# Kernel tuning notes

Hardware: AMD Instinct MI355X
Metric: run time of the kernel (lower is better)

The kernel has to match this reference:

```python
import jax, jax.numpy as jnp
import numpy as np

TEMPERATURE = 1.0
WEIGHT = 1.0


def _transitivity_sum(rel):
    """rel: [N, N] relation probabilities for one (batch, relation) slice.
    Computes sum_{a,b,c} relu(rel[a,b] - rel[a,c] * rel[b,c]) via a scan over c
    (outer product of column c), keeping memory at O(N^2) instead of O(N^3)."""
    def step(acc, col):  # col = rel[:, c], shape [N]
        viol = jax.nn.relu(rel - col[:, None] * col[None, :])  # [N, N]
        return acc + jnp.sum(viol), None
    acc, _ = jax.lax.scan(step, jnp.zeros((), rel.dtype), rel.T)
    return acc


def setup_inputs() -> dict:
    key = jax.random.key(0)
    B, N, R = 2, 512, 4
    relation_logits = jax.random.normal(key, (B, N, N, R), dtype=jnp.float32)
    entity_masks = jnp.ones((B, N), dtype=jnp.int32)
    return {"relation_logits": relation_logits, "entity_masks": entity_masks}


def reference(relation_logits, entity_masks):
    B, N, _, R = relation_logits.shape
    probs = jax.nn.sigmoid(relation_logits / TEMPERATURE)  # [B, N, N, R]
    m = (entity_masks > 0).astype(probs.dtype)             # [B, N]
    rel = probs * m[:, :, None, None] * m[:, None, :, None]
    # flatten (batch, relation) and vmap the per-matrix cubic reduction
    rel_br = jnp.transpose(rel, (0, 3, 1, 2)).reshape(B * R, N, N)
    per = jax.vmap(_transitivity_sum)(rel_br)              # [B*R]
    # per-batch loss = sum_r / R; final = weight * mean over batch
    return WEIGHT * jnp.sum(per) / (R * B)
```

## Files before the change

kernel.cpp:

```cpp
#include <hip/hip_runtime.h>
#include <math.h>

#define N      512
#define RNUM   4
#define BNUM   2
#define NSLICE (RNUM * BNUM)
#define TILE   64
#define CT     64
#define PAD    4
#define STRIDE (TILE + PAD)
#define CSPLIT 2

__device__ __forceinline__ float sigmoidf_(float x) {
  return 1.0f / (1.0f + __expf(-x));
}

__global__ void zero_out_kernel(float* out) { out[0] = 0.0f; }

__global__ __launch_bounds__(256) void prep_kernel(const float* __restrict__ logits,
                                                   const int* __restrict__ masks,
                                                   float* __restrict__ P) {
  int t = blockIdx.x * 256 + threadIdx.x;
  int b = t / (N * N);
  int rem = t - b * (N * N);
  int i = rem / N;
  int j = rem - i * N;
  float4 lg = *(const float4*)(logits + (size_t)t * 4);
  float mm = ((masks[b * N + i] > 0) && (masks[b * N + j] > 0)) ? 1.0f : 0.0f;
  size_t base = (size_t)b * RNUM * N * N + rem;
  P[base + 0 * (size_t)N * N] = mm * sigmoidf_(lg.x);
  P[base + 1 * (size_t)N * N] = mm * sigmoidf_(lg.y);
  P[base + 2 * (size_t)N * N] = mm * sigmoidf_(lg.z);
  P[base + 3 * (size_t)N * N] = mm * sigmoidf_(lg.w);
}

template <bool USE_P>
__global__ __launch_bounds__(256, 4) void trans_main_kernel(const float* __restrict__ P,
                                                            const float* __restrict__ logits,
                                                            const int* __restrict__ masks,
                                                            float* __restrict__ out) {
  const int zz = blockIdx.z;
  const int s  = zz / CSPLIT;
  const int cz = zz % CSPLIT;
  const int a0 = blockIdx.y * TILE;
  const int b0 = blockIdx.x * TILE;
  const int bb = s >> 2;
  const int r  = s & 3;
  const int cbeg = cz * (N / CSPLIT);
  const int cend = cbeg + (N / CSPLIT);

  __shared__ __align__(16) float tA[CT][STRIDE];
  __shared__ __align__(16) float tB[CT][STRIDE];
  __shared__ float wsum[4];

  const int tid = threadIdx.x;
  const int ta  = tid & 15;
  const int tb  = tid >> 4;

  const float* Ps  = P + (size_t)s * N * N;
  const int* mrow  = masks + bb * N;

  float rab[4][4];
  if (USE_P) {
#pragma unroll
    for (int x = 0; x < 4; ++x) {
      float4 rr = *(const float4*)(Ps + (size_t)(a0 + ta * 4 + x) * N + b0 + tb * 4);
      rab[x][0] = rr.x; rab[x][1] = rr.y; rab[x][2] = rr.z; rab[x][3] = rr.w;
    }
  } else {
    float ma[4], mb[4];
#pragma unroll
    for (int x = 0; x < 4; ++x) ma[x] = (mrow[a0 + ta * 4 + x] > 0) ? 1.0f : 0.0f;
#pragma unroll
    for (int y = 0; y < 4; ++y) mb[y] = (mrow[b0 + tb * 4 + y] > 0) ? 1.0f : 0.0f;
#pragma unroll
    for (int x = 0; x < 4; ++x)
#pragma unroll
      for (int y = 0; y < 4; ++y) {
        size_t idx = ((size_t)(bb * N + a0 + ta * 4 + x) * N + (b0 + tb * 4 + y)) * RNUM + r;
        rab[x][y] = sigmoidf_(logits[idx]) * ma[x] * mb[y];
      }
  }

  float acc[4][4];
#pragma unroll
  for (int x = 0; x < 4; ++x)
#pragma unroll
    for (int y = 0; y < 4; ++y) acc[x][y] = 0.0f;

  for (int c0 = cbeg; c0 < cend; c0 += CT) {
    __syncthreads();
    if (USE_P) {
#pragma unroll
      for (int it = 0; it < 4; ++it) {
        int f  = it * 256 + tid;
        int c4 = f & 15;
        int i  = f >> 4;
        int pcol = (((i >> 2) ^ c4) << 2) | (i & 3);
        float4 va = *(const float4*)(Ps + (size_t)(a0 + i) * N + c0 + c4 * 4);
        tA[c4 * 4 + 0][pcol] = va.x;
        tA[c4 * 4 + 1][pcol] = va.y;
        tA[c4 * 4 + 2][pcol] = va.z;
        tA[c4 * 4 + 3][pcol] = va.w;
        float4 vb = *(const float4*)(Ps + (size_t)(b0 + i) * N + c0 + c4 * 4);
        tB[c4 * 4 + 0][pcol] = vb.x;
        tB[c4 * 4 + 1][pcol] = vb.y;
        tB[c4 * 4 + 2][pcol] = vb.z;
        tB[c4 * 4 + 3][pcol] = vb.w;
      }
    } else {
#pragma unroll
      for (int it = 0; it < 16; ++it) {
        int e = it * 256 + tid;
        int c = e & 63;
        int i = e >> 6;
        int pcol = (((i >> 2) ^ ((c >> 2) & 15)) << 2) | (i & 3);
        float mc = (mrow[c0 + c] > 0) ? 1.0f : 0.0f;
        {
          float mi = (mrow[a0 + i] > 0) ? 1.0f : 0.0f;
          size_t idx = ((size_t)(bb * N + a0 + i) * N + (c0 + c)) * RNUM + r;
          tA[c][pcol] = sigmoidf_(logits[idx]) * mi * mc;
        }
        {
          float mi = (mrow[b0 + i] > 0) ? 1.0f : 0.0f;
          size_t idx = ((size_t)(bb * N + b0 + i) * N + (c0 + c)) * RNUM + r;
          tB[c][pcol] = sigmoidf_(logits[idx]) * mi * mc;
        }
      }
    }
    __syncthreads();

#pragma unroll 4
    for (int cg = 0; cg < CT / 4; ++cg) {
      const float* pa = &tA[cg * 4][(ta ^ cg) << 2];
      const float* pb = &tB[cg * 4][(tb ^ cg) << 2];
#pragma unroll
      for (int dc = 0; dc < 4; ++dc) {
        float4 va4 = *(const float4*)(pa + dc * STRIDE);
        float4 vb4 = *(const float4*)(pb + dc * STRIDE);
        float av[4] = {va4.x, va4.y, va4.z, va4.w};
        float bv[4] = {vb4.x, vb4.y, vb4.z, vb4.w};
#pragma unroll
        for (int x = 0; x < 4; ++x)
#pragma unroll
          for (int y = 0; y < 4; ++y) {
            float v = fmaf(-av[x], bv[y], rab[x][y]);
            acc[x][y] += fmaxf(v, 0.0f);
          }
      }
    }
  }

  float tsum = 0.0f;
#pragma unroll
  for (int x = 0; x < 4; ++x)
#pragma unroll
    for (int y = 0; y < 4; ++y) tsum += acc[x][y];

  for (int off = 32; off > 0; off >>= 1) tsum += __shfl_down(tsum, off, 64);

  const int wid  = tid >> 6;
  const int lane = tid & 63;
  if (lane == 0) wsum[wid] = tsum;
  __syncthreads();
  if (tid == 0) {
    float bsum = wsum[0] + wsum[1] + wsum[2] + wsum[3];
    atomicAdd(out, bsum * 0.125f);
  }
}

extern "C" void kernel_launch(void* const* d_in, const int* in_sizes, int n_in,
                              void* d_out, int out_size, void* d_ws, size_t ws_size,
                              hipStream_t stream) {
  const float* logits = (const float*)d_in[0];
  const int*   masks  = (const int*)d_in[1];
  float*       out    = (float*)d_out;

  const size_t P_BYTES = (size_t)NSLICE * N * N * sizeof(float);

  zero_out_kernel<<<1, 1, 0, stream>>>(out);

  dim3 grid(N / TILE, N / TILE, NSLICE * CSPLIT);
  if (ws_size >= P_BYTES) {
    float* P = (float*)d_ws;
    prep_kernel<<<(BNUM * N * N) / 256, 256, 0, stream>>>(logits, masks, P);
    trans_main_kernel<true><<<grid, 256, 0, stream>>>(P, logits, masks, out);
  } else {
    trans_main_kernel<false><<<grid, 256, 0, stream>>>(nullptr, logits, masks, out);
  }
}
```

Measured before the change: 137.8 us.

## Rewrite relu sum as abs plus closed-form column sums, enlarge register tile

Uses relu(v) = (v + |v|)/2. The linear part reduces to a closed form over column sums, sum_c S_c(N - S_c), which sixteen extra blocks compute in the same launch. The cubic loop then only accumulates |fma|, and the abs can fold into the add as a source modifier, removing a max instruction per element. Tiles grow to 128x128 with 8x8 register blocking per thread and a 4-way c-split, raising arithmetic intensity per LDS load. Zeroing of the output is folded into the prep kernel to drop one launch. The cost is higher register pressure (occupancy hint lowered to 3) and a different floating-point summation order.

```diff
diff --git a/kernel.cpp b/kernel.cpp
--- a/kernel.cpp
+++ b/kernel.cpp
@@ -5,11 +5,13 @@
 #define RNUM   4
 #define BNUM   2
 #define NSLICE (RNUM * BNUM)
-#define TILE   64
-#define CT     64
+#define TILE   128
+#define CT     32
 #define PAD    4
 #define STRIDE (TILE + PAD)
-#define CSPLIT 2
+#define CSPLIT 4
+#define NCOLB  16
+#define SCALE  0.0625f
 
 __device__ __forceinline__ float sigmoidf_(float x) {
   return 1.0f / (1.0f + __expf(-x));
@@ -19,7 +21,9 @@
 
 __global__ __launch_bounds__(256) void prep_kernel(const float* __restrict__ logits,
                                                    const int* __restrict__ masks,
-                                                   float* __restrict__ P) {
+                                                   float* __restrict__ P,
+                                                   float* __restrict__ out) {
+  if (blockIdx.x == 0 && threadIdx.x == 0) out[0] = 0.0f;
   int t = blockIdx.x * 256 + threadIdx.x;
   int b = t / (N * N);
   int rem = t - b * (N * N);
@@ -35,58 +39,96 @@
 }
 
 template <bool USE_P>
-__global__ __launch_bounds__(256, 4) void trans_main_kernel(const float* __restrict__ P,
-                                                            const float* __restrict__ logits,
-                                                            const int* __restrict__ masks,
-                                                            float* __restrict__ out) {
-  const int zz = blockIdx.z;
-  const int s  = zz / CSPLIT;
-  const int cz = zz % CSPLIT;
-  const int a0 = blockIdx.y * TILE;
-  const int b0 = blockIdx.x * TILE;
+__global__ __launch_bounds__(256, 3) void work_kernel(const float* __restrict__ P,
+                                                      const float* __restrict__ logits,
+                                                      const int* __restrict__ masks,
+                                                      float* __restrict__ out) {
+  __shared__ __align__(16) float tA[CT][STRIDE];
+  __shared__ __align__(16) float tB[CT][STRIDE];
+  __shared__ float wsum[4];
+
+  const int tid = threadIdx.x;
+  const int bid = blockIdx.x;
+
+  if (bid < NCOLB) {
+    const int s    = bid >> 1;
+    const int half = bid & 1;
+    const int c    = half * 256 + tid;
+    const int bb   = s >> 2;
+    const int r    = s & 3;
+    float sum = 0.0f;
+    if (USE_P) {
+      const float* Ps = P + (size_t)s * N * N + c;
+#pragma unroll 8
+      for (int a = 0; a < N; ++a) sum += Ps[(size_t)a * N];
+    } else {
+      const int* mrow = masks + bb * N;
+      float mc = (mrow[c] > 0) ? 1.0f : 0.0f;
+#pragma unroll 4
+      for (int a = 0; a < N; ++a) {
+        float ma = (mrow[a] > 0) ? 1.0f : 0.0f;
+        size_t idx = ((size_t)(bb * N + a) * N + c) * RNUM + r;
+        sum += sigmoidf_(logits[idx]) * ma * mc;
+      }
+    }
+    float v = sum * ((float)N - sum);
+    for (int off = 32; off > 0; off >>= 1) v += __shfl_down(v, off, 64);
+    const int wid = tid >> 6;
+    if ((tid & 63) == 0) wsum[wid] = v;
+    __syncthreads();
+    if (tid == 0)
+      atomicAdd(out, (wsum[0] + wsum[1] + wsum[2] + wsum[3]) * SCALE);
+    return;
+  }
+
+  const int m  = bid - NCOLB;
+  const int bt = m & 3;
+  const int at = (m >> 2) & 3;
+  const int s  = (m >> 4) & 7;
+  const int cz = m >> 7;
+  const int a0 = at * TILE;
+  const int b0 = bt * TILE;
   const int bb = s >> 2;
   const int r  = s & 3;
   const int cbeg = cz * (N / CSPLIT);
   const int cend = cbeg + (N / CSPLIT);
 
-  __shared__ __align__(16) float tA[CT][STRIDE];
-  __shared__ __align__(16) float tB[CT][STRIDE];
-  __shared__ float wsum[4];
-
-  const int tid = threadIdx.x;
-  const int ta  = tid & 15;
-  const int tb  = tid >> 4;
-
-  const float* Ps  = P + (size_t)s * N * N;
-  const int* mrow  = masks + bb * N;
-
-  float rab[4][4];
+  const int ta = tid & 15;
+  const int tb = tid >> 4;
+
+  const float* Ps = P + (size_t)s * N * N;
+  const int* mrow = masks + bb * N;
+
+  float rab[8][8];
   if (USE_P) {
 #pragma unroll
-    for (int x = 0; x < 4; ++x) {
-      float4 rr = *(const float4*)(Ps + (size_t)(a0 + ta * 4 + x) * N + b0 + tb * 4);
-      rab[x][0] = rr.x; rab[x][1] = rr.y; rab[x][2] = rr.z; rab[x][3] = rr.w;
+    for (int x = 0; x < 8; ++x) {
+      int ra = a0 + ((x >> 2) << 6) + ta * 4 + (x & 3);
+      float4 r0 = *(const float4*)(Ps + (size_t)ra * N + b0 + tb * 4);
+      float4 r1 = *(const float4*)(Ps + (size_t)ra * N + b0 + 64 + tb * 4);
+      rab[x][0] = r0.x; rab[x][1] = r0.y; rab[x][2] = r0.z; rab[x][3] = r0.w;
+      rab[x][4] = r1.x; rab[x][5] = r1.y; rab[x][6] = r1.z; rab[x][7] = r1.w;
     }
   } else {
-    float ma[4], mb[4];
-#pragma unroll
-    for (int x = 0; x < 4; ++x) ma[x] = (mrow[a0 + ta * 4 + x] > 0) ? 1.0f : 0.0f;
-#pragma unroll
-    for (int y = 0; y < 4; ++y) mb[y] = (mrow[b0 + tb * 4 + y] > 0) ? 1.0f : 0.0f;
-#pragma unroll
-    for (int x = 0; x < 4; ++x)
-#pragma unroll
-      for (int y = 0; y < 4; ++y) {
-        size_t idx = ((size_t)(bb * N + a0 + ta * 4 + x) * N + (b0 + tb * 4 + y)) * RNUM + r;
-        rab[x][y] = sigmoidf_(logits[idx]) * ma[x] * mb[y];
-      }
-  }
-
-  float acc[4][4];
-#pragma unroll
-  for (int x = 0; x < 4; ++x)
-#pragma unroll
-    for (int y = 0; y < 4; ++y) acc[x][y] = 0.0f;
+#pragma unroll
+    for (int x = 0; x < 8; ++x) {
+      int ra = a0 + ((x >> 2) << 6) + ta * 4 + (x & 3);
+      float ma = (mrow[ra] > 0) ? 1.0f : 0.0f;
+#pragma unroll
+      for (int y = 0; y < 8; ++y) {
+        int cbcol = b0 + ((y >> 2) << 6) + tb * 4 + (y & 3);
+        float mb = (mrow[cbcol] > 0) ? 1.0f : 0.0f;
+        size_t idx = ((size_t)(bb * N + ra) * N + cbcol) * RNUM + r;
+        rab[x][y] = sigmoidf_(logits[idx]) * ma * mb;
+      }
+    }
+  }
+
+  float acc[8][8];
+#pragma unroll
+  for (int x = 0; x < 8; ++x)
+#pragma unroll
+    for (int y = 0; y < 8; ++y) acc[x][y] = 0.0f;
 
   for (int c0 = cbeg; c0 < cend; c0 += CT) {
     __syncthreads();
@@ -94,79 +136,77 @@
 #pragma unroll
       for (int it = 0; it < 4; ++it) {
         int f  = it * 256 + tid;
-        int c4 = f & 15;
-        int i  = f >> 4;
-        int pcol = (((i >> 2) ^ c4) << 2) | (i & 3);
+        int c4 = f & 7;
+        int i  = f >> 3;
+        int pc = ((((i >> 2) ^ c4) & 31) << 2) | (i & 3);
         float4 va = *(const float4*)(Ps + (size_t)(a0 + i) * N + c0 + c4 * 4);
-        tA[c4 * 4 + 0][pcol] = va.x;
-        tA[c4 * 4 + 1][pcol] = va.y;
-        tA[c4 * 4 + 2][pcol] = va.z;
-        tA[c4 * 4 + 3][pcol] = va.w;
+        tA[c4 * 4 + 0][pc] = va.x;
+        tA[c4 * 4 + 1][pc] = va.y;
+        tA[c4 * 4 + 2][pc] = va.z;
+        tA[c4 * 4 + 3][pc] = va.w;
         float4 vb = *(const float4*)(Ps + (size_t)(b0 + i) * N + c0 + c4 * 4);
-        tB[c4 * 4 + 0][pcol] = vb.x;
-        tB[c4 * 4 + 1][pcol] = vb.y;
-        tB[c4 * 4 + 2][pcol] = vb.z;
-        tB[c4 * 4 + 3][pcol] = vb.w;
+        tB[c4 * 4 + 0][pc] = vb.x;
+        tB[c4 * 4 + 1][pc] = vb.y;
+        tB[c4 * 4 + 2][pc] = vb.z;
+        tB[c4 * 4 + 3][pc] = vb.w;
       }
     } else {
 #pragma unroll
       for (int it = 0; it < 16; ++it) {
         int e = it * 256 + tid;
-        int c = e & 63;
-        int i = e >> 6;
-        int pcol = (((i >> 2) ^ ((c >> 2) & 15)) << 2) | (i & 3);
+        int c = e & 31;
+        int i = e >> 5;
+        int c4 = c >> 2;
+        int pc = ((((i >> 2) ^ c4) & 31) << 2) | (i & 3);
         float mc = (mrow[c0 + c] > 0) ? 1.0f : 0.0f;
         {
           float mi = (mrow[a0 + i] > 0) ? 1.0f : 0.0f;
           size_t idx = ((size_t)(bb * N + a0 + i) * N + (c0 + c)) * RNUM + r;
-          tA[c][pcol] = sigmoidf_(logits[idx]) * mi * mc;
+          tA[c][pc] = sigmoidf_(logits[idx]) * mi * mc;
         }
         {
           float mi = (mrow[b0 + i] > 0) ? 1.0f : 0.0f;
           size_t idx = ((size_t)(bb * N + b0 + i) * N + (c0 + c)) * RNUM + r;
-          tB[c][pcol] = sigmoidf_(logits[idx]) * mi * mc;
+          tB[c][pc] = sigmoidf_(logits[idx]) * mi * mc;
         }
       }
     }
     __syncthreads();
 
-#pragma unroll 4
+#pragma unroll 2
     for (int cg = 0; cg < CT / 4; ++cg) {
-      const float* pa = &tA[cg * 4][(ta ^ cg) << 2];
-      const float* pb = &tB[cg * 4][(tb ^ cg) << 2];
+      const float* pa = &tA[cg * 4][((ta ^ cg) & 31) << 2];
+      const float* pb = &tB[cg * 4][((tb ^ cg) & 31) << 2];
 #pragma unroll
       for (int dc = 0; dc < 4; ++dc) {
-        float4 va4 = *(const float4*)(pa + dc * STRIDE);
-        float4 vb4 = *(const float4*)(pb + dc * STRIDE);
-        float av[4] = {va4.x, va4.y, va4.z, va4.w};
-        float bv[4] = {vb4.x, vb4.y, vb4.z, vb4.w};
-#pragma unroll
-        for (int x = 0; x < 4; ++x)
-#pragma unroll
-          for (int y = 0; y < 4; ++y) {
-            float v = fmaf(-av[x], bv[y], rab[x][y]);
-            acc[x][y] += fmaxf(v, 0.0f);
-          }
+        float4 a0v = *(const float4*)(pa + dc * STRIDE);
+        float4 a1v = *(const float4*)(pa + dc * STRIDE + 64);
+        float4 b0v = *(const float4*)(pb + dc * STRIDE);
+        float4 b1v = *(const float4*)(pb + dc * STRIDE + 64);
+        float av[8] = {a0v.x, a0v.y, a0v.z, a0v.w, a1v.x, a1v.y, a1v.z, a1v.w};
+        float bv[8] = {b0v.x, b0v.y, b0v.z, b0v.w, b1v.x, b1v.y, b1v.z, b1v.w};
+#pragma unroll
+        for (int x = 0; x < 8; ++x)
+#pragma unroll
+          for (int y = 0; y < 8; ++y)
+            acc[x][y] += fabsf(fmaf(-av[x], bv[y], rab[x][y]));
       }
     }
   }
 
   float tsum = 0.0f;
 #pragma unroll
-  for (int x = 0; x < 4; ++x)
-#pragma unroll
-    for (int y = 0; y < 4; ++y) tsum += acc[x][y];
+  for (int x = 0; x < 8; ++x)
+#pragma unroll
+    for (int y = 0; y < 8; ++y) tsum += acc[x][y];
 
   for (int off = 32; off > 0; off >>= 1) tsum += __shfl_down(tsum, off, 64);
 
-  const int wid  = tid >> 6;
-  const int lane = tid & 63;
-  if (lane == 0) wsum[wid] = tsum;
+  const int wid = tid >> 6;
+  if ((tid & 63) == 0) wsum[wid] = tsum;
   __syncthreads();
-  if (tid == 0) {
-    float bsum = wsum[0] + wsum[1] + wsum[2] + wsum[3];
-    atomicAdd(out, bsum * 0.125f);
-  }
+  if (tid == 0)
+    atomicAdd(out, (wsum[0] + wsum[1] + wsum[2] + wsum[3]) * SCALE);
 }
 
 extern "C" void kernel_launch(void* const* d_in, const int* in_sizes, int n_in,
@@ -177,15 +217,14 @@
   float*       out    = (float*)d_out;
 
   const size_t P_BYTES = (size_t)NSLICE * N * N * sizeof(float);
-
-  zero_out_kernel<<<1, 1, 0, stream>>>(out);
-
-  dim3 grid(N / TILE, N / TILE, NSLICE * CSPLIT);
+  const int nblocks = NCOLB + (N / TILE) * (N / TILE) * NSLICE * CSPLIT;
+
   if (ws_size >= P_BYTES) {
     float* P = (float*)d_ws;
-    prep_kernel<<<(BNUM * N * N) / 256, 256, 0, stream>>>(logits, masks, P);
-    trans_main_kernel<true><<<grid, 256, 0, stream>>>(P, logits, masks, out);
+    prep_kernel<<<(BNUM * N * N) / 256, 256, 0, stream>>>(logits, masks, P, out);
+    work_kernel<true><<<nblocks, 256, 0, stream>>>(P, logits, masks, out);
   } else {
-    trans_main_kernel<false><<<grid, 256, 0, stream>>>(nullptr, logits, masks, out);
-  }
-}
+    zero_out_kernel<<<1, 1, 0, stream>>>(out);
+    work_kernel<false><<<nblocks, 256, 0, stream>>>(nullptr, logits, masks, out);
+  }
+}
```

Result: slower. 225.8 us (+63.8%).
